# Performance work log

Measured on AMD Instinct MI355X. Metric: run time of the kernel, lower is better.

The kernel has to match this reference:

```python
import jax, jax.numpy as jnp
import numpy as np

N = 50000    # total nodes in batched graph
E = 800000   # total edges
G = 512      # number of graphs in batch
R = 19       # num_rels (edge types)
D = 64       # hidden dim (dims = [64,64,64])
EMB = D + 1  # embedding dim after concatenating nucleotide scalar
HID = 128
FP = 166     # fingerprint bits


def setup_inputs() -> dict:
    key = jax.random.key(0)
    ks = jax.random.split(key, 24)
    s = 0.05
    inp = {
        "src": jax.random.randint(ks[0], (E,), 0, N, dtype=jnp.int32),
        "dst": jax.random.randint(ks[1], (E,), 0, N, dtype=jnp.int32),
        "etypes": jax.random.randint(ks[2], (E,), 0, R, dtype=jnp.int32),
        "node2graph": jnp.sort(jax.random.randint(ks[3], (N,), 0, G, dtype=jnp.int32)),
        "nuc": jax.random.uniform(ks[4], (N,), dtype=jnp.float32),
        # RelGraphConv layer 0: in_dim=1 (in-degree feature)
        "W0": jax.random.normal(ks[5], (R, 1, D), jnp.float32) * s,
        "b0": jnp.zeros((D,), jnp.float32),
        "L0": jax.random.normal(ks[6], (1, D), jnp.float32) * s,
        # RelGraphConv layer 1
        "W1": jax.random.normal(ks[7], (R, D, D), jnp.float32) * s,
        "b1": jnp.zeros((D,), jnp.float32),
        "L1": jax.random.normal(ks[8], (D, D), jnp.float32) * s,
        # RelGraphConv layer 2 (output layer, no activation)
        "W2": jax.random.normal(ks[9], (R, D, D), jnp.float32) * s,
        "b2": jnp.zeros((D,), jnp.float32),
        "L2": jax.random.normal(ks[10], (D, D), jnp.float32) * s,
        # GlobalAttentionPooling gate: Linear(EMB, 1)
        "gate_w": jax.random.normal(ks[11], (EMB, 1), jnp.float32) * s,
        "gate_b": jnp.zeros((1,), jnp.float32),
        # Attributor MLP: Linear(65,128)+ReLU, Linear(128,166)+Sigmoid
        "A1": jax.random.normal(ks[12], (EMB, HID), jnp.float32) * s,
        "ab1": jnp.zeros((HID,), jnp.float32),
        "A2": jax.random.normal(ks[13], (HID, FP), jnp.float32) * s,
        "ab2": jnp.zeros((FP,), jnp.float32),
    }
    return inp


def reference(src, dst, etypes, node2graph, nuc,
              W0, b0, L0, W1, b1, L1, W2, b2, L2,
              gate_w, gate_b, A1, ab1, A2, ab2):
    # input feature: in-degree per node, shape [N, 1]
    deg = jax.ops.segment_sum(jnp.ones((E,), jnp.float32), dst, num_segments=N)[:, None]

    def relconv(h, W, L, b, act):
        # per-relation projection of all nodes: [N, R, dout]
        proj = jnp.einsum('nd,rdo->nro', h, W)
        msg = proj[src, etypes]                               # [E, dout] gather
        agg = jax.ops.segment_sum(msg, dst, num_segments=N)   # scatter-sum to dst nodes
        out = agg + h @ L + b                                 # self-loop + bias (DGL defaults)
        return jax.nn.relu(out) if act else out

    h = relconv(deg, W0, L0, b0, True)
    h = relconv(h,   W1, L1, b1, True)
    h = relconv(h,   W2, L2, b2, False)

    # nucs=True: concat nucleotide scalar -> [N, 65]
    emb = jnp.concatenate([h, nuc[:, None]], axis=1)

    # GlobalAttentionPooling: per-graph segment softmax over gate scores
    gate = (emb @ gate_w + gate_b)[:, 0]                       # [N]
    gmax = jax.ops.segment_max(gate, node2graph, num_segments=G)
    ex = jnp.exp(gate - gmax[node2graph])
    denom = jax.ops.segment_sum(ex, node2graph, num_segments=G)
    alpha = ex / denom[node2graph]
    fp = jax.ops.segment_sum(alpha[:, None] * emb, node2graph, num_segments=G)  # [G, 65]

    # Attributor (dropout is identity in eval)
    h1 = jax.nn.relu(fp @ A1 + ab1)
    out = jax.nn.sigmoid(h1 @ A2 + ab2)                        # [G, 166]
    return out, emb
```

## Files before the change

### kernel.cpp

```cpp
#include <hip/hip_runtime.h>
#include <cstdint>

static constexpr int NN = 50000;
static constexpr int NE = 800000;
static constexpr int NG = 512;
static constexpr int NR = 19;
static constexpr int DD = 64;
static constexpr int EMB = 65;
static constexpr int HID = 128;
static constexpr int FP = 166;
static constexpr int NEP = NE + NR * 16;
static constexpr int NMSG = NE + 304;
static constexpr int SCB = (NN + 255) / 256;

typedef __fp16 h2 __attribute__((ext_vector_type(2)));
typedef _Float16 F16x2 __attribute__((ext_vector_type(2)));
typedef _Float16 hf8 __attribute__((ext_vector_type(8)));
typedef float f32x4 __attribute__((ext_vector_type(4)));
typedef unsigned u32x4 __attribute__((ext_vector_type(4)));
typedef int i32x4 __attribute__((ext_vector_type(4)));

union U4H8 { u32x4 u; hf8 h; };

__device__ __forceinline__ hf8 as_hf8(u32x4 u) { U4H8 c; c.u = u; return c.h; }

__device__ __forceinline__ float dot2f(unsigned a, unsigned b, float c) {
    union { unsigned u; h2 h; } ua, ub;
    ua.u = a; ub.u = b;
    return __builtin_amdgcn_fdot2(ua.h, ub.h, c, false);
}

__device__ __forceinline__ unsigned pack2(float a, float b) {
    union { h2 h; unsigned u; } r;
    r.h = __builtin_amdgcn_cvt_pkrtz(a, b);
    return r.u;
}

__device__ __forceinline__ void pkAtomicAdd(unsigned* addr, float lo, float hi) {
    unsigned u = pack2(lo, hi);
#if __has_builtin(__builtin_amdgcn_global_atomic_fadd_v2f16)
    union { unsigned u; F16x2 h; } c; c.u = u;
    __builtin_amdgcn_global_atomic_fadd_v2f16((F16x2*)addr, c.h);
#else
    asm volatile("global_atomic_pk_add_f16 %0, %1, off" :: "v"(addr), "v"(u) : "memory");
#endif
}

__device__ __forceinline__ float half_at(unsigned v, int idx) {
    union { unsigned u; h2 h; } c; c.u = v;
    return (float)c.h[idx];
}

__device__ __forceinline__ int lbound(const int* __restrict__ a, int key) {
    int lo = 0, hi = NN;
    while (lo < hi) {
        int mid = (lo + hi) >> 1;
        if (a[mid] < key) lo = mid + 1; else hi = mid;
    }
    return lo;
}

__global__ __launch_bounds__(256) void khist(const int* __restrict__ dst, int* __restrict__ degi) {
    int e = blockIdx.x * 256 + threadIdx.x;
    if (e < NE) atomicAdd(&degi[dst[e]], 1);
}

__global__ __launch_bounds__(256) void ketcnt(const int* __restrict__ et, int* __restrict__ cnt19) {
    const int lane = threadIdx.x & 63;
    const int wid = threadIdx.x >> 6;
    const int wbase = (blockIdx.x * 4 + wid) * 512;
    int cnt = 0;
#pragma unroll
    for (int i = 0; i < 8; ++i) {
        int e = wbase + i * 64 + lane;
        int myet = (e < NE) ? et[e] : -1;
#pragma unroll
        for (int r = 0; r < NR; ++r) {
            unsigned long long b = __ballot(myet == r);
            if (lane == r) cnt += (int)__popcll(b);
        }
    }
    if (lane < NR && cnt) atomicAdd(&cnt19[lane], cnt);
}

__global__ __launch_bounds__(512) void kprepw(const int* __restrict__ cnt19, int* __restrict__ pbase,
                                              int* __restrict__ cur19, int* __restrict__ batchptr,
                                              unsigned* __restrict__ hpk0, unsigned* __restrict__ hpk1,
                                              unsigned* __restrict__ sdp,
                                              const float* __restrict__ W1, const float* __restrict__ W2,
                                              unsigned* __restrict__ wpk1, unsigned* __restrict__ wpk2) {
    if (blockIdx.x == 0) {
        __shared__ int spb[NR + 1];
        int t = threadIdx.x;
        if (t == 0) {
            int run = 0;
            for (int r = 0; r < NR; ++r) {
                spb[r] = run; pbase[r] = run; cur19[r] = run; batchptr[r] = run >> 4;
                run += (cnt19[r] + 15) & ~15;
            }
            spb[NR] = run; pbase[NR] = run; batchptr[NR] = run >> 4;
        }
        if (t < 32) hpk0[(size_t)NN * 32 + t] = 0;
        else if (t < 64) hpk1[(size_t)NN * 32 + (t - 32)] = 0;
        __syncthreads();
        int r = t >> 4, i = t & 15;
        if (r < NR) {
            int cnt = cnt19[r];
            int tail = spb[r + 1] - spb[r] - cnt;
            if (i < tail) {
                int pos = spb[r] + cnt + i;
                sdp[pos] = (unsigned)NN | ((unsigned)NN << 16);
            }
        }
    } else {
        int t = (blockIdx.x - 1) * 512 + threadIdx.x;
        if (t >= 2 * NR * 8 * 64) return;
        int which = t >= NR * 8 * 64;
        int tt = t - which * NR * 8 * 64;
        const float* W = which ? W2 : W1;
        unsigned* wpk = which ? wpk2 : wpk1;
        int lane = tt & 63;
        int f = (tt >> 6) & 7;
        int r = tt >> 9;
        int kh = f >> 2, ct = f & 3;
        int kbase = kh * 32 + (lane >> 4) * 8;
        int col = (ct >> 1) * 32 + 2 * (lane & 15) + (ct & 1);
        const float* wr = W + (size_t)r * DD * DD;
        u32x4 out;
#pragma unroll
        for (int p = 0; p < 4; ++p)
            out[p] = pack2(wr[(kbase + 2 * p) * DD + col], wr[(kbase + 2 * p + 1) * DD + col]);
        *((u32x4*)wpk + tt) = out;
    }
}

__global__ __launch_bounds__(256) void kscanA(const int* __restrict__ degi, int* __restrict__ part) {
    __shared__ int red[256];
    int t = threadIdx.x, b = blockIdx.x;
    int idx = b * 256 + t;
    red[t] = (idx < NN) ? degi[idx] : 0;
    __syncthreads();
#pragma unroll
    for (int s = 128; s > 0; s >>= 1) {
        if (t < s) red[t] += red[t + s];
        __syncthreads();
    }
    if (t == 0) part[b] = red[0];
}

__global__ __launch_bounds__(256) void kscanBC(const int* __restrict__ degi, const int* __restrict__ part,
                                               int* __restrict__ dstoff, int* __restrict__ cur) {
    __shared__ int sp[256];
    __shared__ int s[256];
    int t = threadIdx.x, b = blockIdx.x;
    sp[t] = (t < SCB) ? part[t] : 0;
    int idx = b * 256 + t;
    int v = (idx < NN) ? degi[idx] : 0;
    s[t] = v;
    __syncthreads();
#pragma unroll
    for (int d = 1; d < 256; d <<= 1) {
        int x1 = (t >= d) ? sp[t - d] : 0;
        int x2 = (t >= d) ? s[t - d] : 0;
        __syncthreads();
        sp[t] += x1;
        s[t] += x2;
        __syncthreads();
    }
    int boff = (b == 0) ? 0 : sp[b - 1];
    int excl = boff + ((t == 0) ? 0 : s[t - 1]);
    if (idx < NN) { dstoff[idx] = excl; cur[idx] = excl; }
    if (idx == NN - 1) { dstoff[NN] = NE; cur[NN] = NE; }
}

__global__ __launch_bounds__(256) void kscatter(const int* __restrict__ src, const int* __restrict__ dst,
                                                const int* __restrict__ et, int* __restrict__ cur19,
                                                unsigned* __restrict__ sdp, unsigned char* __restrict__ ets) {
    __shared__ int wcnt[4][NR];
    __shared__ int lb[NR];
    __shared__ int woff[4][NR];
    const int t = threadIdx.x;
    const int lane = t & 63;
    const int wid = t >> 6;
    int e = blockIdx.x * 256 + t;
    int myet = -1, d = 0, sv = 0;
    if (e < NE) { myet = et[e]; d = dst[e]; sv = src[e]; }
    const unsigned long long below = (lane == 63) ? ~0ull >> 1 : ((1ull << lane) - 1);
    int myrank = 0, cnt_r = 0;
#pragma unroll
    for (int r = 0; r < NR; ++r) {
        unsigned long long m = __ballot(myet == r);
        if (myet == r) myrank = (int)__popcll(m & below);
        if (lane == r) cnt_r = (int)__popcll(m);
    }
    if (lane < NR) wcnt[wid][lane] = cnt_r;
    __syncthreads();
    if (t < NR) {
        int c0 = wcnt[0][t], c1 = wcnt[1][t], c2 = wcnt[2][t], c3 = wcnt[3][t];
        int tot = c0 + c1 + c2 + c3;
        lb[t] = tot ? atomicAdd(&cur19[t], tot) : 0;
        woff[0][t] = 0; woff[1][t] = c0; woff[2][t] = c0 + c1; woff[3][t] = c0 + c1 + c2;
    }
    __syncthreads();
    if (e < NE) {
        int pos = lb[myet] + woff[wid][myet] + myrank;
        sdp[pos] = (unsigned)sv | ((unsigned)d << 16);
        ets[pos] = (unsigned char)myet;
    }
}

__global__ __launch_bounds__(256) void kperm(const unsigned* __restrict__ sdp, const unsigned char* __restrict__ ets,
                                             const int* __restrict__ pbase, const int* __restrict__ degi,
                                             int* __restrict__ cur, int* __restrict__ perm,
                                             unsigned* __restrict__ msg0) {
    int p = blockIdx.x * 256 + threadIdx.x;
    if (p >= pbase[NR]) return;
    unsigned sd = sdp[p];
    int s = (int)(sd & 0xffffu);
    int d = (int)(sd >> 16);
    int deg = (s < NN) ? degi[s] : 0;
    unsigned etv = ets[p];
    int slot = atomicAdd(&cur[d], 1);
    perm[p] = slot;
    msg0[slot] = (etv << 16) | (unsigned)deg;
}

__global__ __launch_bounds__(256) void kf0m(const unsigned* __restrict__ msg0, const int* __restrict__ dstoff,
                                            const float* __restrict__ W0, const float* __restrict__ L0,
                                            const float* __restrict__ b0, unsigned* __restrict__ hpk0) {
    __shared__ float Lw[NR * DD];
    for (int i = threadIdx.x; i < NR * DD; i += 256) Lw[i] = W0[i];
    __syncthreads();
    int lane = threadIdx.x & 63;
    int wid = __builtin_amdgcn_readfirstlane(threadIdx.x >> 6);
    int n = blockIdx.x * 4 + wid;
    if (n >= NN) return;
    int r0 = dstoff[n], r1 = dstoff[n + 1];
    float deg = (float)(r1 - r0);
    float acc = b0[lane] + deg * L0[lane];
    for (int row = r0; row < r1; ++row) {
        unsigned v = msg0[row];
        acc += (float)(v & 0xffffu) * Lw[(v >> 16) * DD + lane];
    }
    acc = fmaxf(acc, 0.f);
    float other = __shfl_xor(acc, 1);
    if ((lane & 1) == 0) hpk0[n * 32 + (lane >> 1)] = pack2(acc, other);
}

__global__ __launch_bounds__(256) void ktpass(const int* __restrict__ src, const int* __restrict__ dst,
                                              const int* __restrict__ et, const int* __restrict__ degi,
                                              float* __restrict__ T) {
    int e = blockIdx.x * 256 + threadIdx.x;
    if (e < NE) unsafeAtomicAdd(&T[dst[e] * NR + et[e]], (float)degi[src[e]]);
}

__global__ __launch_bounds__(256) void kf0(const float* __restrict__ T, const float* __restrict__ W0,
                                           const float* __restrict__ L0, const float* __restrict__ b0,
                                           const int* __restrict__ degi, unsigned* __restrict__ hpk0) {
    int lane = threadIdx.x & 63;
    int wid = __builtin_amdgcn_readfirstlane(threadIdx.x >> 6);
    int n = blockIdx.x * 4 + wid;
    if (n >= NN) return;
    float w0r[NR];
#pragma unroll
    for (int r = 0; r < NR; ++r) w0r[r] = W0[r * DD + lane];
    float acc = b0[lane] + (float)degi[n] * L0[lane];
    const float* Trow = T + n * NR;
#pragma unroll
    for (int r = 0; r < NR; ++r) acc += Trow[r] * w0r[r];
    acc = fmaxf(acc, 0.f);
    float other = __shfl_xor(acc, 1);
    if ((lane & 1) == 0) hpk0[n * 32 + (lane >> 1)] = pack2(acc, other);
}

template <bool STORE>
__global__ __launch_bounds__(256) void kmsgm(const unsigned* __restrict__ sdp, const int* __restrict__ perm,
                                             const int* __restrict__ batchptr, const unsigned* __restrict__ hpk,
                                             const unsigned* __restrict__ wpk, unsigned* __restrict__ out) {
    const int lane = threadIdx.x & 63;
    int wid = __builtin_amdgcn_readfirstlane(threadIdx.x >> 6);
    int gw = blockIdx.x * 4 + wid;
    const int nwaves = gridDim.x * 4;
    const int totB = batchptr[NR];
    int chunk = (totB + nwaves - 1) / nwaves;
    int b0 = gw * chunk;
    int b1 = min(b0 + chunk, totB);
    if (b0 >= b1) return;

    int r = 0;
    while (batchptr[r + 1] <= b0) ++r;

    hf8 Bf[8];
    auto loadB = [&](int rr) {
        const u32x4* wq = (const u32x4*)wpk;
#pragma unroll
        for (int f = 0; f < 8; ++f) Bf[f] = as_hf8(wq[(rr * 8 + f) * 64 + lane]);
    };
    loadB(r);
    int rend = batchptr[r + 1];

    const int qk = lane >> 4;
    const int lm = lane & 15;

    for (int b = b0; b < b1; ++b) {
        while (b >= rend) {
            ++r;
            rend = batchptr[r + 1];
            if (b < rend) loadB(r);
        }
        int base = b << 4;
        int s = (int)(sdp[base + lm] & 0xffffu);
        const unsigned* hr = hpk + (size_t)s * 32;
        hf8 a0 = as_hf8(*(const u32x4*)(hr + (qk << 2)));
        hf8 a1 = as_hf8(*(const u32x4*)(hr + 16 + (qk << 2)));
        i32x4 d4;
        if constexpr (STORE) {
            d4 = *(const i32x4*)(perm + base + (qk << 2));
        } else {
            u32x4 sd4 = *(const u32x4*)(sdp + base + (qk << 2));
#pragma unroll
            for (int j = 0; j < 4; ++j) d4[j] = (int)(sd4[j] >> 16);
        }

        f32x4 acc0 = {0.f, 0.f, 0.f, 0.f};
        f32x4 acc1 = {0.f, 0.f, 0.f, 0.f};
        f32x4 acc2 = {0.f, 0.f, 0.f, 0.f};
        f32x4 acc3 = {0.f, 0.f, 0.f, 0.f};
        acc0 = __builtin_amdgcn_mfma_f32_16x16x32_f16(a0, Bf[0], acc0, 0, 0, 0);
        acc1 = __builtin_amdgcn_mfma_f32_16x16x32_f16(a0, Bf[1], acc1, 0, 0, 0);
        acc2 = __builtin_amdgcn_mfma_f32_16x16x32_f16(a0, Bf[2], acc2, 0, 0, 0);
        acc3 = __builtin_amdgcn_mfma_f32_16x16x32_f16(a0, Bf[3], acc3, 0, 0, 0);
        acc0 = __builtin_amdgcn_mfma_f32_16x16x32_f16(a1, Bf[4], acc0, 0, 0, 0);
        acc1 = __builtin_amdgcn_mfma_f32_16x16x32_f16(a1, Bf[5], acc1, 0, 0, 0);
        acc2 = __builtin_amdgcn_mfma_f32_16x16x32_f16(a1, Bf[6], acc2, 0, 0, 0);
        acc3 = __builtin_amdgcn_mfma_f32_16x16x32_f16(a1, Bf[7], acc3, 0, 0, 0);

#pragma unroll
        for (int j = 0; j < 4; ++j) {
            if constexpr (STORE) {
                unsigned pk0 = pack2(acc0[j], acc1[j]);
                unsigned pk1 = pack2(acc2[j], acc3[j]);
                unsigned long long v = ((unsigned long long)pk1 << 32) | pk0;
                *(unsigned long long*)(out + (size_t)d4[j] * 32 + 2 * lm) = v;
            } else {
                unsigned* ag = out + (size_t)d4[j] * 32 + lm;
                pkAtomicAdd(ag, acc0[j], acc1[j]);
                pkAtomicAdd(ag + 16, acc2[j], acc3[j]);
            }
        }
    }
}

template <bool ACT, bool WRITE_EMB, bool MSGMODE>
__global__ __launch_bounds__(256) void kfin(const unsigned* __restrict__ agm, const int* __restrict__ dstoff,
                                            const unsigned* __restrict__ hpk_in, const float* __restrict__ L,
                                            const float* __restrict__ bvec, unsigned* __restrict__ hpk_out,
                                            float* __restrict__ embp, const float* __restrict__ nuc,
                                            const float* __restrict__ gatew, const float* __restrict__ gateb,
                                            float* __restrict__ gate) {
    __shared__ unsigned Lp[32 * 64];
    for (int i = threadIdx.x; i < 2048; i += 256) {
        int kp = i >> 6, o = i & 63;
        Lp[i] = pack2(L[(2 * kp) * DD + o], L[(2 * kp + 1) * DD + o]);
    }
    __syncthreads();
    int lane = threadIdx.x & 63;
    int wid = __builtin_amdgcn_readfirstlane(threadIdx.x >> 6);
    int n = blockIdx.x * 4 + wid;
    if (n >= NN) return;
    float acc = bvec[lane];
    if constexpr (MSGMODE) {
        const int dwp = lane & 15;
        const int ro = lane >> 4;
        int r0 = dstoff[n], r1 = dstoff[n + 1];
        float m0a = 0.f, m1a = 0.f, m2a = 0.f, m3a = 0.f;
        for (int row = r0; row < r1; row += 4) {
            int rr = row + ro;
            unsigned long long v = 0;
            if (rr < r1) v = *(const unsigned long long*)(agm + (size_t)rr * 32 + 2 * dwp);
            unsigned vlo = (unsigned)v, vhi = (unsigned)(v >> 32);
            m0a += half_at(vlo, 0); m1a += half_at(vlo, 1);
            m2a += half_at(vhi, 0); m3a += half_at(vhi, 1);
        }
        m0a += __shfl_xor(m0a, 16); m0a += __shfl_xor(m0a, 32);
        m1a += __shfl_xor(m1a, 16); m1a += __shfl_xor(m1a, 32);
        m2a += __shfl_xor(m2a, 16); m2a += __shfl_xor(m2a, 32);
        m3a += __shfl_xor(m3a, 16); m3a += __shfl_xor(m3a, 32);
        int dp = (lane & 31) >> 1;
        float s0 = __shfl(m0a, dp), s1 = __shfl(m1a, dp);
        float s2 = __shfl(m2a, dp), s3 = __shfl(m3a, dp);
        float sel_lo = (lane & 1) ? s1 : s0;
        float sel_hi = (lane & 1) ? s3 : s2;
        acc += (lane >= 32) ? sel_hi : sel_lo;
    } else {
        acc += half_at(agm[(size_t)n * 32 + (lane >> 1)], lane & 1);
    }
    const unsigned* hr = hpk_in + n * 32;
    float a0 = 0.f, a1 = 0.f, a2 = 0.f, a3 = 0.f;
#pragma unroll
    for (int k4 = 0; k4 < 8; ++k4) {
        a0 = dot2f(hr[4 * k4 + 0], Lp[(4 * k4 + 0) * 64 + lane], a0);
        a1 = dot2f(hr[4 * k4 + 1], Lp[(4 * k4 + 1) * 64 + lane], a1);
        a2 = dot2f(hr[4 * k4 + 2], Lp[(4 * k4 + 2) * 64 + lane], a2);
        a3 = dot2f(hr[4 * k4 + 3], Lp[(4 * k4 + 3) * 64 + lane], a3);
    }
    acc += (a0 + a1) + (a2 + a3);
    if (ACT) acc = fmaxf(acc, 0.f);
    if constexpr (WRITE_EMB) {
        embp[(size_t)n * EMB + lane] = acc;
        float nv = nuc[n];
        if (lane == 0) embp[(size_t)n * EMB + 64] = nv;
        float v = acc * gatew[lane];
#pragma unroll
        for (int s = 32; s >= 1; s >>= 1) v += __shfl_xor(v, s);
        if (lane == 0) gate[n] = v + nv * gatew[64] + gateb[0];
    } else {
        float other = __shfl_xor(acc, 1);
        if ((lane & 1) == 0) hpk_out[n * 32 + (lane >> 1)] = pack2(acc, other);
    }
}

__global__ __launch_bounds__(128) void kpool(const int* __restrict__ n2g, const float* __restrict__ gate,
                                             const float* __restrict__ emb, float* __restrict__ fpb) {
    __shared__ float red[128];
    __shared__ float c64[2];
    int g = blockIdx.x;
    int t = threadIdx.x;
    int lo = lbound(n2g, g);
    int hi = lbound(n2g, g + 1);

    float m = -INFINITY;
    for (int i = lo + t; i < hi; i += 128) m = fmaxf(m, gate[i]);
    red[t] = m;
    __syncthreads();
    for (int s = 64; s > 0; s >>= 1) {
        if (t < s) red[t] = fmaxf(red[t], red[t + s]);
        __syncthreads();
    }
    m = red[0];
    __syncthreads();

    float sum = 0.f;
    for (int i = lo + t; i < hi; i += 128) sum += __expf(gate[i] - m);
    red[t] = sum;
    __syncthreads();
    for (int s = 64; s > 0; s >>= 1) {
        if (t < s) red[t] += red[t + s];
        __syncthreads();
    }
    float denom = red[0];
    __syncthreads();

    const int lane = t & 63;
    const int wv = t >> 6;
    float acc = 0.f, acc64 = 0.f;
    for (int i = lo + wv; i < hi; i += 2) {
        float wt = __expf(gate[i] - m);
        acc += wt * emb[(size_t)i * EMB + lane];
        if (lane == 0) acc64 += wt * emb[(size_t)i * EMB + 64];
    }
    red[t] = acc;
    if (lane == 0) c64[wv] = acc64;
    __syncthreads();
    if (t < 64) {
        float s = red[t] + red[64 + t];
        fpb[g * EMB + t] = (hi > lo) ? s / denom : 0.f;
    } else if (t == 64) {
        float s = c64[0] + c64[1];
        fpb[g * EMB + 64] = (hi > lo) ? s / denom : 0.f;
    }
}

__global__ __launch_bounds__(128) void kmlp(const float* __restrict__ fpb, const float* __restrict__ A1,
                                            const float* __restrict__ ab1, const float* __restrict__ A2,
                                            const float* __restrict__ ab2, float* __restrict__ out) {
    __shared__ float fv[EMB];
    __shared__ float h1[HID];
    int g = blockIdx.x;
    int t = threadIdx.x;
    if (t < EMB) fv[t] = fpb[g * EMB + t];
    __syncthreads();
    float a = ab1[t];
    for (int d = 0; d < EMB; ++d) a += fv[d] * A1[d * HID + t];
    h1[t] = fmaxf(a, 0.f);
    __syncthreads();
    for (int o = t; o < FP; o += HID) {
        float v = ab2[o];
        for (int k = 0; k < HID; ++k) v += h1[k] * A2[k * FP + o];
        out[(size_t)g * FP + o] = 1.f / (1.f + __expf(-v));
    }
}

extern "C" void kernel_launch(void* const* d_in, const int* in_sizes, int n_in,
                              void* d_out, int out_size, void* d_ws, size_t ws_size,
                              hipStream_t stream) {
    const int* src = (const int*)d_in[0];
    const int* dst = (const int*)d_in[1];
    const int* et = (const int*)d_in[2];
    const int* n2g = (const int*)d_in[3];
    const float* nuc = (const float*)d_in[4];
    const float* W0 = (const float*)d_in[5];
    const float* b0 = (const float*)d_in[6];
    const float* L0 = (const float*)d_in[7];
    const float* W1 = (const float*)d_in[8];
    const float* b1 = (const float*)d_in[9];
    const float* L1 = (const float*)d_in[10];
    const float* W2 = (const float*)d_in[11];
    const float* b2 = (const float*)d_in[12];
    const float* L2 = (const float*)d_in[13];
    const float* gatew = (const float*)d_in[14];
    const float* gateb = (const float*)d_in[15];
    const float* A1 = (const float*)d_in[16];
    const float* ab1 = (const float*)d_in[17];
    const float* A2 = (const float*)d_in[18];
    const float* ab2 = (const float*)d_in[19];
    (void)in_sizes; (void)n_in; (void)out_size;

    float* out0 = (float*)d_out;
    float* embp = (float*)d_out + (size_t)NG * FP;

    char* w = (char*)d_ws;
    size_t off = 0;
    auto alloc = [&](size_t bytes) { size_t r = off; off = (off + bytes + 255) & ~(size_t)255; return r; };

    size_t o_degi = alloc(NN * 4);
    size_t o_cnt  = alloc(NR * 4);
    size_t zero_small = off;
    size_t o_T    = alloc((size_t)NN * NR * 4);
    size_t zero_big = off;
    size_t o_hpk0 = alloc((size_t)(NN + 1) * 32 * 4);
    size_t o_hpk1 = alloc((size_t)(NN + 1) * 32 * 4);
    size_t o_pb   = alloc((NR + 1) * 4);
    size_t o_cur19= alloc(NR * 4);
    size_t o_bp   = alloc((NR + 1) * 4);
    size_t o_sdp  = alloc((size_t)NEP * 4);
    size_t o_ets  = alloc((size_t)NEP);
    size_t o_perm = alloc((size_t)NEP * 4);
    size_t o_msg0 = alloc((size_t)NMSG * 4);
    size_t o_doff = alloc((size_t)(NN + 1) * 4);
    size_t o_cur  = alloc((size_t)(NN + 1) * 4);
    size_t o_part = alloc((size_t)SCB * 4);
    size_t o_wpk1 = alloc((size_t)NR * 8 * 64 * 16);
    size_t o_wpk2 = alloc((size_t)NR * 8 * 64 * 16);
    size_t o_gate = alloc(NN * 4);
    size_t o_fpb  = alloc((size_t)NG * EMB * 4);
    size_t o_msg  = off;
    size_t need_store = o_msg + (size_t)NMSG * 128;
    bool use_store = ws_size >= need_store;

    int* degi = (int*)(w + o_degi);
    int* cnt19 = (int*)(w + o_cnt);
    float* T = (float*)(w + o_T);
    unsigned* hpk0 = (unsigned*)(w + o_hpk0);
    unsigned* hpk1 = (unsigned*)(w + o_hpk1);
    int* pbase = (int*)(w + o_pb);
    int* cur19 = (int*)(w + o_cur19);
    int* batchptr = (int*)(w + o_bp);
    unsigned* sdp = (unsigned*)(w + o_sdp);
    unsigned char* ets = (unsigned char*)(w + o_ets);
    int* perm = (int*)(w + o_perm);
    unsigned* msg0 = (unsigned*)(w + o_msg0);
    int* dstoff = (int*)(w + o_doff);
    int* cur = (int*)(w + o_cur);
    int* part = (int*)(w + o_part);
    unsigned* wpk1 = (unsigned*)(w + o_wpk1);
    unsigned* wpk2 = (unsigned*)(w + o_wpk2);
    float* gate = (float*)(w + o_gate);
    float* fpb = (float*)(w + o_fpb);
    unsigned* msg = (unsigned*)(w + o_msg);

    const int EB  = (NE + 255) / 256;
    const int EB8 = (NE + 2047) / 2048;
    const int EBP = (NEP + 255) / 256;
    const int NW  = (NN + 3) / 4;
    const int WPB512 = (2 * NR * 8 * 64 + 511) / 512;

    hipMemsetAsync(w, 0, use_store ? zero_small : zero_big, stream);

    khist<<<EB, 256, 0, stream>>>(dst, degi);
    ketcnt<<<EB8, 256, 0, stream>>>(et, cnt19);
    kprepw<<<1 + WPB512, 512, 0, stream>>>(cnt19, pbase, cur19, batchptr, hpk0, hpk1,
                                           sdp, W1, W2, wpk1, wpk2);
    kscatter<<<EB, 256, 0, stream>>>(src, dst, et, cur19, sdp, ets);

    if (use_store) {
        kscanA<<<SCB, 256, 0, stream>>>(degi, part);
        kscanBC<<<SCB, 256, 0, stream>>>(degi, part, dstoff, cur);
        kperm<<<EBP, 256, 0, stream>>>(sdp, ets, pbase, degi, cur, perm, msg0);
        kf0m<<<NW, 256, 0, stream>>>(msg0, dstoff, W0, L0, b0, hpk0);

        kmsgm<true><<<1024, 256, 0, stream>>>(sdp, perm, batchptr, hpk0, wpk1, msg);
        kfin<true, false, true><<<NW, 256, 0, stream>>>(msg, dstoff, hpk0, L1, b1, hpk1,
                                                        nullptr, nullptr, nullptr, nullptr, nullptr);
        kmsgm<true><<<1024, 256, 0, stream>>>(sdp, perm, batchptr, hpk1, wpk2, msg);
        kfin<false, true, true><<<NW, 256, 0, stream>>>(msg, dstoff, hpk1, L2, b2, nullptr,
                                                        embp, nuc, gatew, gateb, gate);
    } else {
        ktpass<<<EB, 256, 0, stream>>>(src, dst, et, degi, T);
        kf0<<<NW, 256, 0, stream>>>(T, W0, L0, b0, degi, hpk0);
        hipMemsetAsync(msg, 0, (size_t)NN * 32 * 4, stream);
        kmsgm<false><<<1024, 256, 0, stream>>>(sdp, nullptr, batchptr, hpk0, wpk1, msg);
        kfin<true, false, false><<<NW, 256, 0, stream>>>(msg, nullptr, hpk0, L1, b1, hpk1,
                                                         nullptr, nullptr, nullptr, nullptr, nullptr);
        hipMemsetAsync(msg, 0, (size_t)NN * 32 * 4, stream);
        kmsgm<false><<<1024, 256, 0, stream>>>(sdp, nullptr, batchptr, hpk1, wpk2, msg);
        kfin<false, true, false><<<NW, 256, 0, stream>>>(msg, nullptr, hpk1, L2, b2, nullptr,
                                                         embp, nuc, gatew, gateb, gate);
    }

    kpool<<<NG, 128, 0, stream>>>(n2g, gate, embp, fpb);
    kmlp<<<NG, 128, 0, stream>>>(fpb, A1, ab1, A2, ab2, out0);
}
```

Measured before the change: 350.8 us.

## Merge independent preprocessing kernels into combined launches and fuse pool with MLP

Packs independent preprocessing stages into shared grids. The histogram and edge-type count run as one launch. The scan partials and the weight packing run as another. The prefix scan and the edge-type scatter run as a third. All three use 512-thread blocks, and the global attention pooling kernel is fused with the attributor MLP. This removes four kernel launches and the intermediate fp buffer round trip, which targets launch and serialization overhead across a long chain of small kernels. In exchange, the scan now uses 512-wide blocks, the scatter uses 8 waves per block, and padding slots also get an ets entry written.

```diff
diff --git a/kernel.cpp b/kernel.cpp
--- a/kernel.cpp
+++ b/kernel.cpp
@@ -11,7 +11,10 @@
 static constexpr int FP = 166;
 static constexpr int NEP = NE + NR * 16;
 static constexpr int NMSG = NE + 304;
-static constexpr int SCB = (NN + 255) / 256;
+static constexpr int SCB5 = (NN + 511) / 512;
+static constexpr int EB5  = (NE + 511) / 512;
+static constexpr int ET5  = (NE + 4095) / 4096;
+static constexpr int WPB512 = (2 * NR * 8 * 64 + 511) / 512;
 
 typedef __fp16 h2 __attribute__((ext_vector_type(2)));
 typedef _Float16 F16x2 __attribute__((ext_vector_type(2)));
@@ -60,38 +63,55 @@
     return lo;
 }
 
-__global__ __launch_bounds__(256) void khist(const int* __restrict__ dst, int* __restrict__ degi) {
-    int e = blockIdx.x * 256 + threadIdx.x;
-    if (e < NE) atomicAdd(&degi[dst[e]], 1);
-}
-
-__global__ __launch_bounds__(256) void ketcnt(const int* __restrict__ et, int* __restrict__ cnt19) {
-    const int lane = threadIdx.x & 63;
-    const int wid = threadIdx.x >> 6;
-    const int wbase = (blockIdx.x * 4 + wid) * 512;
-    int cnt = 0;
-#pragma unroll
-    for (int i = 0; i < 8; ++i) {
-        int e = wbase + i * 64 + lane;
-        int myet = (e < NE) ? et[e] : -1;
-#pragma unroll
-        for (int r = 0; r < NR; ++r) {
-            unsigned long long b = __ballot(myet == r);
-            if (lane == r) cnt += (int)__popcll(b);
-        }
-    }
-    if (lane < NR && cnt) atomicAdd(&cnt19[lane], cnt);
-}
-
-__global__ __launch_bounds__(512) void kprepw(const int* __restrict__ cnt19, int* __restrict__ pbase,
-                                              int* __restrict__ cur19, int* __restrict__ batchptr,
-                                              unsigned* __restrict__ hpk0, unsigned* __restrict__ hpk1,
-                                              unsigned* __restrict__ sdp,
-                                              const float* __restrict__ W1, const float* __restrict__ W2,
-                                              unsigned* __restrict__ wpk1, unsigned* __restrict__ wpk2) {
-    if (blockIdx.x == 0) {
+__global__ __launch_bounds__(512) void kd1(const int* __restrict__ dst, const int* __restrict__ et,
+                                           int* __restrict__ degi, int* __restrict__ cnt19) {
+    const int b = blockIdx.x;
+    const int t = threadIdx.x;
+    if (b < EB5) {
+        int e = b * 512 + t;
+        if (e < NE) atomicAdd(&degi[dst[e]], 1);
+    } else {
+        const int bb = b - EB5;
+        const int lane = t & 63;
+        const int wid = t >> 6;
+        const int wbase = (bb * 8 + wid) * 512;
+        int cnt = 0;
+#pragma unroll
+        for (int i = 0; i < 8; ++i) {
+            int e = wbase + i * 64 + lane;
+            int myet = (e < NE) ? et[e] : -1;
+#pragma unroll
+            for (int r = 0; r < NR; ++r) {
+                unsigned long long bm = __ballot(myet == r);
+                if (lane == r) cnt += (int)__popcll(bm);
+            }
+        }
+        if (lane < NR && cnt) atomicAdd(&cnt19[lane], cnt);
+    }
+}
+
+__global__ __launch_bounds__(512) void kd2(const int* __restrict__ degi, int* __restrict__ part,
+                                           const int* __restrict__ cnt19, int* __restrict__ pbase,
+                                           int* __restrict__ cur19, int* __restrict__ batchptr,
+                                           unsigned* __restrict__ hpk0, unsigned* __restrict__ hpk1,
+                                           unsigned* __restrict__ sdp, unsigned char* __restrict__ ets,
+                                           const float* __restrict__ W1, const float* __restrict__ W2,
+                                           unsigned* __restrict__ wpk1, unsigned* __restrict__ wpk2) {
+    const int b = blockIdx.x;
+    const int t = threadIdx.x;
+    if (b < SCB5) {
+        __shared__ int red[512];
+        int idx = b * 512 + t;
+        red[t] = (idx < NN) ? degi[idx] : 0;
+        __syncthreads();
+#pragma unroll
+        for (int s = 256; s > 0; s >>= 1) {
+            if (t < s) red[t] += red[t + s];
+            __syncthreads();
+        }
+        if (t == 0) part[b] = red[0];
+    } else if (b == SCB5) {
         __shared__ int spb[NR + 1];
-        int t = threadIdx.x;
         if (t == 0) {
             int run = 0;
             for (int r = 0; r < NR; ++r) {
@@ -110,18 +130,19 @@
             if (i < tail) {
                 int pos = spb[r] + cnt + i;
                 sdp[pos] = (unsigned)NN | ((unsigned)NN << 16);
+                ets[pos] = 0;
             }
         }
     } else {
-        int t = (blockIdx.x - 1) * 512 + threadIdx.x;
-        if (t >= 2 * NR * 8 * 64) return;
-        int which = t >= NR * 8 * 64;
-        int tt = t - which * NR * 8 * 64;
+        int tt = (b - SCB5 - 1) * 512 + t;
+        if (tt >= 2 * NR * 8 * 64) return;
+        int which = tt >= NR * 8 * 64;
+        int t2 = tt - which * NR * 8 * 64;
         const float* W = which ? W2 : W1;
         unsigned* wpk = which ? wpk2 : wpk1;
-        int lane = tt & 63;
-        int f = (tt >> 6) & 7;
-        int r = tt >> 9;
+        int lane = t2 & 63;
+        int f = (t2 >> 6) & 7;
+        int r = t2 >> 9;
         int kh = f >> 2, ct = f & 3;
         int kbase = kh * 32 + (lane >> 4) * 8;
         int col = (ct >> 1) * 32 + 2 * (lane & 15) + (ct & 1);
@@ -130,82 +151,72 @@
 #pragma unroll
         for (int p = 0; p < 4; ++p)
             out[p] = pack2(wr[(kbase + 2 * p) * DD + col], wr[(kbase + 2 * p + 1) * DD + col]);
-        *((u32x4*)wpk + tt) = out;
-    }
-}
-
-__global__ __launch_bounds__(256) void kscanA(const int* __restrict__ degi, int* __restrict__ part) {
-    __shared__ int red[256];
-    int t = threadIdx.x, b = blockIdx.x;
-    int idx = b * 256 + t;
-    red[t] = (idx < NN) ? degi[idx] : 0;
-    __syncthreads();
-#pragma unroll
-    for (int s = 128; s > 0; s >>= 1) {
-        if (t < s) red[t] += red[t + s];
+        *((u32x4*)wpk + t2) = out;
+    }
+}
+
+__global__ __launch_bounds__(512) void kd3(const int* __restrict__ degi, const int* __restrict__ part,
+                                           int* __restrict__ dstoff, int* __restrict__ cur,
+                                           const int* __restrict__ src, const int* __restrict__ dst,
+                                           const int* __restrict__ et, int* __restrict__ cur19,
+                                           unsigned* __restrict__ sdp, unsigned char* __restrict__ ets) {
+    const int b = blockIdx.x;
+    const int t = threadIdx.x;
+    if (b < SCB5) {
+        __shared__ int sp[512];
+        __shared__ int s[512];
+        sp[t] = (t < SCB5) ? part[t] : 0;
+        int idx = b * 512 + t;
+        int v = (idx < NN) ? degi[idx] : 0;
+        s[t] = v;
         __syncthreads();
-    }
-    if (t == 0) part[b] = red[0];
-}
-
-__global__ __launch_bounds__(256) void kscanBC(const int* __restrict__ degi, const int* __restrict__ part,
-                                               int* __restrict__ dstoff, int* __restrict__ cur) {
-    __shared__ int sp[256];
-    __shared__ int s[256];
-    int t = threadIdx.x, b = blockIdx.x;
-    sp[t] = (t < SCB) ? part[t] : 0;
-    int idx = b * 256 + t;
-    int v = (idx < NN) ? degi[idx] : 0;
-    s[t] = v;
-    __syncthreads();
-#pragma unroll
-    for (int d = 1; d < 256; d <<= 1) {
-        int x1 = (t >= d) ? sp[t - d] : 0;
-        int x2 = (t >= d) ? s[t - d] : 0;
+#pragma unroll
+        for (int d = 1; d < 512; d <<= 1) {
+            int x1 = (t >= d) ? sp[t - d] : 0;
+            int x2 = (t >= d) ? s[t - d] : 0;
+            __syncthreads();
+            sp[t] += x1;
+            s[t] += x2;
+            __syncthreads();
+        }
+        int boff = (b == 0) ? 0 : sp[b - 1];
+        int excl = boff + ((t == 0) ? 0 : s[t - 1]);
+        if (idx < NN) { dstoff[idx] = excl; cur[idx] = excl; }
+        if (idx == NN - 1) { dstoff[NN] = NE; cur[NN] = NE; }
+    } else {
+        __shared__ int wcnt[8][NR];
+        __shared__ int lb[NR];
+        __shared__ int woff[8][NR];
+        const int bb = b - SCB5;
+        const int lane = t & 63;
+        const int wid = t >> 6;
+        int e = bb * 512 + t;
+        int myet = -1, d = 0, sv = 0;
+        if (e < NE) { myet = et[e]; d = dst[e]; sv = src[e]; }
+        const unsigned long long below = (lane == 63) ? ~0ull >> 1 : ((1ull << lane) - 1);
+        int myrank = 0, cnt_r = 0;
+#pragma unroll
+        for (int r = 0; r < NR; ++r) {
+            unsigned long long m = __ballot(myet == r);
+            if (myet == r) myrank = (int)__popcll(m & below);
+            if (lane == r) cnt_r = (int)__popcll(m);
+        }
+        if (lane < NR) wcnt[wid][lane] = cnt_r;
         __syncthreads();
-        sp[t] += x1;
-        s[t] += x2;
+        if (t < NR) {
+            int run = 0, c[8];
+#pragma unroll
+            for (int wv = 0; wv < 8; ++wv) { c[wv] = wcnt[wv][t]; }
+#pragma unroll
+            for (int wv = 0; wv < 8; ++wv) { woff[wv][t] = run; run += c[wv]; }
+            lb[t] = run ? atomicAdd(&cur19[t], run) : 0;
+        }
         __syncthreads();
-    }
-    int boff = (b == 0) ? 0 : sp[b - 1];
-    int excl = boff + ((t == 0) ? 0 : s[t - 1]);
-    if (idx < NN) { dstoff[idx] = excl; cur[idx] = excl; }
-    if (idx == NN - 1) { dstoff[NN] = NE; cur[NN] = NE; }
-}
-
-__global__ __launch_bounds__(256) void kscatter(const int* __restrict__ src, const int* __restrict__ dst,
-                                                const int* __restrict__ et, int* __restrict__ cur19,
-                                                unsigned* __restrict__ sdp, unsigned char* __restrict__ ets) {
-    __shared__ int wcnt[4][NR];
-    __shared__ int lb[NR];
-    __shared__ int woff[4][NR];
-    const int t = threadIdx.x;
-    const int lane = t & 63;
-    const int wid = t >> 6;
-    int e = blockIdx.x * 256 + t;
-    int myet = -1, d = 0, sv = 0;
-    if (e < NE) { myet = et[e]; d = dst[e]; sv = src[e]; }
-    const unsigned long long below = (lane == 63) ? ~0ull >> 1 : ((1ull << lane) - 1);
-    int myrank = 0, cnt_r = 0;
-#pragma unroll
-    for (int r = 0; r < NR; ++r) {
-        unsigned long long m = __ballot(myet == r);
-        if (myet == r) myrank = (int)__popcll(m & below);
-        if (lane == r) cnt_r = (int)__popcll(m);
-    }
-    if (lane < NR) wcnt[wid][lane] = cnt_r;
-    __syncthreads();
-    if (t < NR) {
-        int c0 = wcnt[0][t], c1 = wcnt[1][t], c2 = wcnt[2][t], c3 = wcnt[3][t];
-        int tot = c0 + c1 + c2 + c3;
-        lb[t] = tot ? atomicAdd(&cur19[t], tot) : 0;
-        woff[0][t] = 0; woff[1][t] = c0; woff[2][t] = c0 + c1; woff[3][t] = c0 + c1 + c2;
-    }
-    __syncthreads();
-    if (e < NE) {
-        int pos = lb[myet] + woff[wid][myet] + myrank;
-        sdp[pos] = (unsigned)sv | ((unsigned)d << 16);
-        ets[pos] = (unsigned char)myet;
+        if (e < NE) {
+            int pos = lb[myet] + woff[wid][myet] + myrank;
+            sdp[pos] = (unsigned)sv | ((unsigned)d << 16);
+            ets[pos] = (unsigned char)myet;
+        }
     }
 }
 
@@ -420,10 +431,14 @@
     }
 }
 
-__global__ __launch_bounds__(128) void kpool(const int* __restrict__ n2g, const float* __restrict__ gate,
-                                             const float* __restrict__ emb, float* __restrict__ fpb) {
+__global__ __launch_bounds__(128) void kpoolmlp(const int* __restrict__ n2g, const float* __restrict__ gate,
+                                                const float* __restrict__ emb, const float* __restrict__ A1,
+                                                const float* __restrict__ ab1, const float* __restrict__ A2,
+                                                const float* __restrict__ ab2, float* __restrict__ out) {
     __shared__ float red[128];
     __shared__ float c64[2];
+    __shared__ float fv[EMB];
+    __shared__ float h1[HID];
     int g = blockIdx.x;
     int t = threadIdx.x;
     int lo = lbound(n2g, g);
@@ -464,22 +479,13 @@
     __syncthreads();
     if (t < 64) {
         float s = red[t] + red[64 + t];
-        fpb[g * EMB + t] = (hi > lo) ? s / denom : 0.f;
+        fv[t] = (hi > lo) ? s / denom : 0.f;
     } else if (t == 64) {
         float s = c64[0] + c64[1];
-        fpb[g * EMB + 64] = (hi > lo) ? s / denom : 0.f;
-    }
-}
-
-__global__ __launch_bounds__(128) void kmlp(const float* __restrict__ fpb, const float* __restrict__ A1,
-                                            const float* __restrict__ ab1, const float* __restrict__ A2,
-                                            const float* __restrict__ ab2, float* __restrict__ out) {
-    __shared__ float fv[EMB];
-    __shared__ float h1[HID];
-    int g = blockIdx.x;
-    int t = threadIdx.x;
-    if (t < EMB) fv[t] = fpb[g * EMB + t];
-    __syncthreads();
+        fv[64] = (hi > lo) ? s / denom : 0.f;
+    }
+    __syncthreads();
+
     float a = ab1[t];
     for (int d = 0; d < EMB; ++d) a += fv[d] * A1[d * HID + t];
     h1[t] = fmaxf(a, 0.f);
@@ -539,11 +545,10 @@
     size_t o_msg0 = alloc((size_t)NMSG * 4);
     size_t o_doff = alloc((size_t)(NN + 1) * 4);
     size_t o_cur  = alloc((size_t)(NN + 1) * 4);
-    size_t o_part = alloc((size_t)SCB * 4);
+    size_t o_part = alloc((size_t)SCB5 * 4);
     size_t o_wpk1 = alloc((size_t)NR * 8 * 64 * 16);
     size_t o_wpk2 = alloc((size_t)NR * 8 * 64 * 16);
     size_t o_gate = alloc(NN * 4);
-    size_t o_fpb  = alloc((size_t)NG * EMB * 4);
     size_t o_msg  = off;
     size_t need_store = o_msg + (size_t)NMSG * 128;
     bool use_store = ws_size >= need_store;
@@ -566,26 +571,20 @@
     unsigned* wpk1 = (unsigned*)(w + o_wpk1);
     unsigned* wpk2 = (unsigned*)(w + o_wpk2);
     float* gate = (float*)(w + o_gate);
-    float* fpb = (float*)(w + o_fpb);
     unsigned* msg = (unsigned*)(w + o_msg);
 
     const int EB  = (NE + 255) / 256;
-    const int EB8 = (NE + 2047) / 2048;
     const int EBP = (NEP + 255) / 256;
     const int NW  = (NN + 3) / 4;
-    const int WPB512 = (2 * NR * 8 * 64 + 511) / 512;
 
     hipMemsetAsync(w, 0, use_store ? zero_small : zero_big, stream);
 
-    khist<<<EB, 256, 0, stream>>>(dst, degi);
-    ketcnt<<<EB8, 256, 0, stream>>>(et, cnt19);
-    kprepw<<<1 + WPB512, 512, 0, stream>>>(cnt19, pbase, cur19, batchptr, hpk0, hpk1,
-                                           sdp, W1, W2, wpk1, wpk2);
-    kscatter<<<EB, 256, 0, stream>>>(src, dst, et, cur19, sdp, ets);
+    kd1<<<EB5 + ET5, 512, 0, stream>>>(dst, et, degi, cnt19);
+    kd2<<<SCB5 + 1 + WPB512, 512, 0, stream>>>(degi, part, cnt19, pbase, cur19, batchptr,
+                                               hpk0, hpk1, sdp, ets, W1, W2, wpk1, wpk2);
+    kd3<<<SCB5 + EB5, 512, 0, stream>>>(degi, part, dstoff, cur, src, dst, et, cur19, sdp, ets);
 
     if (use_store) {
-        kscanA<<<SCB, 256, 0, stream>>>(degi, part);
-        kscanBC<<<SCB, 256, 0, stream>>>(degi, part, dstoff, cur);
         kperm<<<EBP, 256, 0, stream>>>(sdp, ets, pbase, degi, cur, perm, msg0);
         kf0m<<<NW, 256, 0, stream>>>(msg0, dstoff, W0, L0, b0, hpk0);
 
@@ -608,6 +607,5 @@
                                                          embp, nuc, gatew, gateb, gate);
     }
 
-    kpool<<<NG, 128, 0, stream>>>(n2g, gate, embp, fpb);
-    kmlp<<<NG, 128, 0, stream>>>(fpb, A1, ab1, A2, ab2, out0);
-}
+    kpoolmlp<<<NG, 128, 0, stream>>>(n2g, gate, embp, A1, ab1, A2, ab2, out0);
+}
```

Result: faster. 314.9 us (-10.2%).
